# Optimization experiments

Measured on AMD Instinct MI355X. Metric: run time of the kernel, lower is better.

## Reference

```python
import jax, jax.numpy as jnp
import numpy as np

N, E = 50000, 800000
D_IN, D_HID, D_OUT = 128, 128, 64


def sage_conv(x, src, dst, w_l, w_r, b, n_nodes):
    # PyG SAGEConv (aggr='mean', root_weight=True):
    #   out = lin_l(mean_{j in N(i)} x_j) + lin_r(x_i)
    msg_sum = jax.ops.segment_sum(x[src], dst, num_segments=n_nodes)  # [N, d]
    cnt = jax.ops.segment_sum(jnp.ones((src.shape[0],), x.dtype), dst,
                              num_segments=n_nodes)                   # [N]
    mean = msg_sum / jnp.maximum(cnt, 1.0)[:, None]
    return mean @ w_l.T + x @ w_r.T + b


def prelu(x, a):
    return jnp.maximum(x, 0) + a * jnp.minimum(x, 0)


def setup_inputs() -> dict:
    key = jax.random.key(0)
    ks = jax.random.split(key, 12)
    def lin(k, o, i):
        s = 1.0 / np.sqrt(i)
        return jax.random.uniform(k, (o, i), jnp.float32, -s, s)
    x = jax.random.normal(ks[0], (N, D_IN), jnp.float32)
    edge_index = jax.random.randint(ks[1], (2, E), 0, N, jnp.int64)
    return {
        "x": x,
        "edge_index": edge_index,
        "w1l": lin(ks[2], D_HID, D_IN),  "w1r": lin(ks[3], D_HID, D_IN),
        "b1": jnp.zeros((D_HID,), jnp.float32),
        "w2l": lin(ks[4], D_HID, D_HID), "w2r": lin(ks[5], D_HID, D_HID),
        "b2": jnp.zeros((D_HID,), jnp.float32),
        "w3l": lin(ks[6], D_OUT, D_HID), "w3r": lin(ks[7], D_OUT, D_HID),
        "b3": jnp.zeros((D_OUT,), jnp.float32),
        "a": jnp.array(0.25, jnp.float32),  # shared PReLU slope
        "wp": lin(ks[8], 1, D_OUT),
        "bp": jnp.zeros((1,), jnp.float32),
    }


def reference(x, edge_index, w1l, w1r, b1, w2l, w2r, b2, w3l, w3r, b3, a, wp, bp):
    src, dst = edge_index[0], edge_index[1]
    n = x.shape[0]
    h = prelu(sage_conv(x, src, dst, w1l, w1r, b1, n), a)
    h = prelu(sage_conv(h, src, dst, w2l, w2r, b2, n), a)
    h = sage_conv(h, src, dst, w3l, w3r, b3, n)          # [N, D_OUT]
    level = (h @ wp.T + bp).squeeze(-1)                  # [N]
    return level
```

## Files before the change

### kernel.cpp

```cpp
#include <hip/hip_runtime.h>
#include <cstdint>
#include <cstddef>

typedef float f32x4 __attribute__((ext_vector_type(4)));
typedef short short8 __attribute__((ext_vector_type(8)));
typedef __bf16 bf16x8 __attribute__((ext_vector_type(8)));

__device__ __forceinline__ void mfma_bf16(f32x4& d, short8 a, short8 b){
  d = __builtin_amdgcn_mfma_f32_16x16x32_bf16(
        __builtin_bit_cast(bf16x8, a), __builtin_bit_cast(bf16x8, b), d, 0, 0, 0);
}

__device__ __forceinline__ unsigned short bf16_rn(float f){
  unsigned u = __float_as_uint(f);
  unsigned r = (u + 0x7FFF + ((u >> 16) & 1)) >> 16;
  return (unsigned short)r;
}

__device__ __forceinline__ int blockScan256Excl(int v, int* wsum){
  const int lane = threadIdx.x & 63, wv = threadIdx.x >> 6;
  int x = v;
  #pragma unroll
  for (int off = 1; off < 64; off <<= 1){
    int y = __shfl_up(x, off);
    if (lane >= off) x += y;
  }
  if (lane == 63) wsum[wv] = x;
  __syncthreads();
  int woff = 0;
  #pragma unroll
  for (int w = 0; w < 4; ++w) woff += (w < wv) ? wsum[w] : 0;
  return woff + x - v;
}

__global__ __launch_bounds__(256) void k_bcount(const int* __restrict__ dst, int E, int nb, int ntiles,
                                                int* __restrict__ blk_hist){
  __shared__ int h[256];
  const int tile = blockIdx.x;
  h[threadIdx.x] = 0;
  __syncthreads();
  const int base = tile * 2048;
  const int end = min(base + 2048, E);
  for (int i = base + threadIdx.x; i < end; i += 256)
    atomicAdd(&h[dst[i] >> 8], 1);
  __syncthreads();
  const int b = threadIdx.x;
  if (b < nb) blk_hist[(size_t)b * ntiles + tile] = h[b];
}

__global__ __launch_bounds__(256) void k_bscan(int* __restrict__ blk_hist, int nb, int ntiles,
                                               int* __restrict__ tot){
  __shared__ int wsum[4];
  __shared__ int carry;
  const int b = blockIdx.x;
  int* row = blk_hist + (size_t)b * ntiles;
  if (threadIdx.x == 0) carry = 0;
  __syncthreads();
  const int lane = threadIdx.x & 63, wv = threadIdx.x >> 6;
  for (int base = 0; base < ntiles; base += 256){
    const int i = base + threadIdx.x;
    const int v = (i < ntiles) ? row[i] : 0;
    int x = v;
    #pragma unroll
    for (int off = 1; off < 64; off <<= 1){
      int y = __shfl_up(x, off);
      if (lane >= off) x += y;
    }
    if (lane == 63) wsum[wv] = x;
    __syncthreads();
    int woff = 0;
    #pragma unroll
    for (int w = 0; w < 4; ++w) woff += (w < wv) ? wsum[w] : 0;
    const int incl = carry + woff + x;
    if (i < ntiles) row[i] = incl - v;
    __syncthreads();
    if (threadIdx.x == 255) carry = incl;
    __syncthreads();
  }
  if (threadIdx.x == 0) tot[b] = carry;
}

__global__ __launch_bounds__(256) void k_btot(const int* __restrict__ tot, int nb,
                                              int* __restrict__ bucket_base){
  __shared__ int wsum[4];
  const int t = threadIdx.x;
  const int v = (t < nb) ? tot[t] : 0;
  const int e = blockScan256Excl(v, wsum);
  if (t <= nb) bucket_base[t] = e;
}

__global__ __launch_bounds__(256) void k_bscat(const int* __restrict__ src, const int* __restrict__ dst,
                                               int E, int nb, int ntiles,
                                               const int* __restrict__ blk_off,
                                               const int* __restrict__ bucket_base,
                                               unsigned* __restrict__ ebuf){
  __shared__ int cnt[256];
  __shared__ int lofs[256];
  __shared__ int gbase[256];
  __shared__ unsigned sorted[2048];
  __shared__ unsigned char sb[2048];
  __shared__ int wsum[4];
  const int tile = blockIdx.x;
  cnt[threadIdx.x] = 0;
  __syncthreads();
  const int base = tile * 2048;
  const int end = min(base + 2048, E);
  const int m = end - base;

  int rank_[8]; int b_[8]; unsigned v_[8];
  #pragma unroll
  for (int k = 0; k < 8; ++k){
    const int j = threadIdx.x + k * 256;
    if (base + j < end){
      const int d = dst[base + j];
      const int s = src[base + j];
      const int b = d >> 8;
      b_[k] = b;
      v_[k] = ((unsigned)(d & 255) << 16) | (unsigned)s;
      rank_[k] = atomicAdd(&cnt[b], 1);
    } else b_[k] = -1;
  }
  __syncthreads();
  const int ex = blockScan256Excl(cnt[threadIdx.x], wsum);
  lofs[threadIdx.x] = ex;
  if (threadIdx.x < nb)
    gbase[threadIdx.x] = bucket_base[threadIdx.x] + blk_off[(size_t)threadIdx.x * ntiles + tile];
  __syncthreads();
  #pragma unroll
  for (int k = 0; k < 8; ++k){
    if (b_[k] >= 0){
      const int p = lofs[b_[k]] + rank_[k];
      sorted[p] = v_[k];
      sb[p] = (unsigned char)b_[k];
    }
  }
  __syncthreads();
  for (int j = threadIdx.x; j < m; j += 256){
    const int b = sb[j];
    ebuf[gbase[b] + (j - lofs[b])] = sorted[j];
  }
}

__global__ __launch_bounds__(256) void k_csrfin(const unsigned* __restrict__ ebuf,
                                                const int* __restrict__ bucket_base,
                                                int n, int E, int nb,
                                                int* __restrict__ row_ptr,
                                                float* __restrict__ inv,
                                                unsigned short* __restrict__ csr){
  __shared__ int hist[256], excl[256], cursor[256];
  __shared__ int wsum[4];
  __shared__ unsigned vals[8192];
  __shared__ unsigned short sorted[8192];
  const int b = blockIdx.x;
  const int ebase = bucket_base[b];
  const int ecnt = bucket_base[b + 1] - ebase;
  const int t = threadIdx.x;
  hist[t] = 0;
  __syncthreads();
  for (int j = t; j < ecnt; j += 256){
    const unsigned v = ebuf[ebase + j];
    vals[j] = v;
    atomicAdd(&hist[v >> 16], 1);
  }
  __syncthreads();
  const int ex = blockScan256Excl(hist[t], wsum);
  excl[t] = ex;
  cursor[t] = ex;
  const int node = b * 256 + t;
  if (node < n){
    row_ptr[node] = ebase + ex;
    const int c = hist[t];
    inv[node] = 1.0f / (float)(c > 0 ? c : 1);
  }
  if (b == nb - 1 && t == 0) row_ptr[n] = E;
  __syncthreads();
  for (int j = t; j < ecnt; j += 256){
    const unsigned v = vals[j];
    const int pos = atomicAdd(&cursor[v >> 16], 1);
    sorted[pos] = (unsigned short)(v & 0xFFFFu);
  }
  __syncthreads();
  for (int j = t; j < ecnt; j += 256)
    csr[ebase + j] = sorted[j];
}

__device__ __forceinline__ void wcs_body(const float* __restrict__ wl, const float* __restrict__ wr,
                                         short* __restrict__ bfr, int id){
  if (id >= 128 * 256) return;
  int c = id >> 8, k = id & 255;
  float w = (k < 128) ? wl[c * 128 + k] : wr[c * 128 + (k - 128)];
  unsigned short h = bf16_rn(w);
  float hf = __uint_as_float((unsigned)h << 16);
  unsigned short l = bf16_rn(w - hf);
  const int nt = c >> 4, mrow = c & 15;
  const int ks = k >> 5, kgrp = (k >> 3) & 3, j = k & 7;
  const int lane = kgrp * 16 + mrow;
  const size_t fbase = (size_t)((ks * 8 + nt) * 2) * 512 + lane * 8 + j;
  bfr[fbase] = (short)h;
  bfr[fbase + 512] = (short)l;
}

__global__ __launch_bounds__(256) void k_prep(const float* __restrict__ x,
                                              unsigned short* __restrict__ xb, int n,
                                              const float* __restrict__ w1l, const float* __restrict__ w1r,
                                              short* __restrict__ bfr1,
                                              const float* __restrict__ w2l, const float* __restrict__ w2r,
                                              short* __restrict__ bfr2,
                                              const float* __restrict__ w3l, const float* __restrict__ w3r,
                                              const float* __restrict__ b3,
                                              const float* __restrict__ wp, const float* __restrict__ bp,
                                              float* __restrict__ u){
  const int nbcvt = (n * 128 / 4 + 255) / 256;
  const int b = blockIdx.x;
  if (b < nbcvt){
    const int i = (b * 256 + threadIdx.x) * 4;
    if (i < n * 128){
      const float4 v = *(const float4*)&x[i];
      ushort2 a, c;
      a.x = bf16_rn(v.x); a.y = bf16_rn(v.y);
      c.x = bf16_rn(v.z); c.y = bf16_rn(v.w);
      *(ushort2*)&xb[i] = a;
      *(ushort2*)&xb[i + 2] = c;
    }
  } else if (b < nbcvt + 128){
    wcs_body(w1l, w1r, bfr1, (b - nbcvt) * 256 + threadIdx.x);
  } else if (b < nbcvt + 256){
    wcs_body(w2l, w2r, bfr2, (b - nbcvt - 128) * 256 + threadIdx.x);
  } else {
    const int k = threadIdx.x;
    if (k < 128){
      float sl = 0.f, sr = 0.f;
      for (int o = 0; o < 64; ++o){
        float w = wp[o];
        sl = fmaf(w, w3l[o * 128 + k], sl);
        sr = fmaf(w, w3r[o * 128 + k], sr);
      }
      u[k] = sl; u[128 + k] = sr;
      if (k == 0){
        float c = bp[0];
        for (int o = 0; o < 64; ++o) c = fmaf(wp[o], b3[o], c);
        u[256] = c;
      }
    }
  }
}

__global__ __launch_bounds__(256) void k_aggb(const unsigned short* __restrict__ featb,
                                              const unsigned short* __restrict__ csr,
                                              const int* __restrict__ row_ptr,
                                              const float* __restrict__ inv_cnt,
                                              unsigned short* __restrict__ outb, int n){
  const int lane = threadIdx.x & 63;
  const int node = (blockIdx.x * blockDim.x + threadIdx.x) >> 6;
  if (node >= n) return;
  const int beg = __builtin_amdgcn_readfirstlane(row_ptr[node]);
  const int end = __builtin_amdgcn_readfirstlane(row_ptr[node + 1]);
  const unsigned* __restrict__ fb = (const unsigned*)featb;

  float axs[8] = {0,0,0,0,0,0,0,0};
  float ays[8] = {0,0,0,0,0,0,0,0};

  int j = beg;
  for (; j + 16 <= end; j += 16){
    unsigned uu[16];
    #pragma unroll
    for (int q = 0; q < 16; ++q) uu[q] = fb[(size_t)csr[j + q] * 64 + lane];
    #pragma unroll
    for (int q = 0; q < 16; ++q){
      axs[q & 7] += __uint_as_float(uu[q] << 16);
      ays[q & 7] += __uint_as_float(uu[q] & 0xFFFF0000u);
    }
  }
  if (j + 8 <= end){
    unsigned uu[8];
    #pragma unroll
    for (int q = 0; q < 8; ++q) uu[q] = fb[(size_t)csr[j + q] * 64 + lane];
    #pragma unroll
    for (int q = 0; q < 8; ++q){
      axs[q] += __uint_as_float(uu[q] << 16);
      ays[q] += __uint_as_float(uu[q] & 0xFFFF0000u);
    }
    j += 8;
  }
  if (j + 4 <= end){
    unsigned uu[4];
    #pragma unroll
    for (int q = 0; q < 4; ++q) uu[q] = fb[(size_t)csr[j + q] * 64 + lane];
    #pragma unroll
    for (int q = 0; q < 4; ++q){
      axs[q] += __uint_as_float(uu[q] << 16);
      ays[q] += __uint_as_float(uu[q] & 0xFFFF0000u);
    }
    j += 4;
  }
  for (; j < end; ++j){
    const unsigned u = fb[(size_t)csr[j] * 64 + lane];
    axs[4] += __uint_as_float(u << 16);
    ays[4] += __uint_as_float(u & 0xFFFF0000u);
  }

  const float ic = inv_cnt[node];
  const float ox = (((axs[0] + axs[1]) + (axs[2] + axs[3])) + ((axs[4] + axs[5]) + (axs[6] + axs[7]))) * ic;
  const float oy = (((ays[0] + ays[1]) + (ays[2] + ays[3])) + ((ays[4] + ays[5]) + (ays[6] + ays[7]))) * ic;
  const unsigned packed = (unsigned)bf16_rn(ox) | ((unsigned)bf16_rn(oy) << 16);
  ((unsigned*)outb)[(size_t)node * 64 + lane] = packed;
}

__global__ __launch_bounds__(256) void k_gemm_mfma(const unsigned short* __restrict__ A0b,
                                                   const unsigned short* __restrict__ A1b,
                                                   const short* __restrict__ bfr,
                                                   const float* __restrict__ bias,
                                                   const float* __restrict__ alpha_p,
                                                   unsigned short* __restrict__ out16,
                                                   const float* __restrict__ uvec,
                                                   float* __restrict__ sbuf,
                                                   float* __restrict__ pbuf,
                                                   int n){
  __shared__ short aT[2][64 * 128];
  const int t = threadIdx.x;
  const int lane = t & 63;
  const int wv = t >> 6;
  const int nodeBase = blockIdx.x * 64;

  #pragma unroll
  for (int tab = 0; tab < 2; ++tab){
    const unsigned short* __restrict__ src = tab ? A1b : A0b;
    #pragma unroll
    for (int it = 0; it < 4; ++it){
      const int chunk = it * 256 + t;
      const int row = chunk >> 4;
      const int slot = chunk & 15;
      int gr = nodeBase + row; if (gr > n - 1) gr = n - 1;
      const uint4 v = *(const uint4*)&src[(size_t)gr * 128 + slot * 8];
      const int sslot = slot ^ (row & 7);
      *(uint4*)((char*)&aT[tab][0] + row * 256 + sslot * 16) = v;
    }
  }
  __syncthreads();

  const short8* __restrict__ Bf = (const short8*)bfr;
  const int mrow = lane & 15;
  const int kgrp = lane >> 4;
  const int arow = wv * 16 + mrow;

  f32x4 acc[8];
  #pragma unroll
  for (int i = 0; i < 8; ++i) acc[i] = (f32x4){0.f, 0.f, 0.f, 0.f};

  #pragma unroll
  for (int ks = 0; ks < 8; ++ks){
    const int tab = ks >> 2;
    const int slot_r = (ks & 3) * 4 + kgrp;
    const short8 aF = *(const short8*)((const char*)&aT[tab][0] + arow * 256 + (slot_r ^ (arow & 7)) * 16);

    short8 bh[8], bl[8];
    const int fb = ks * 16;
    #pragma unroll
    for (int nt = 0; nt < 8; ++nt){
      bh[nt] = Bf[(size_t)(fb + nt * 2 + 0) * 64 + lane];
      bl[nt] = Bf[(size_t)(fb + nt * 2 + 1) * 64 + lane];
    }
    #pragma unroll
    for (int nt = 0; nt < 8; ++nt){
      mfma_bf16(acc[nt], aF, bh[nt]);
      mfma_bf16(acc[nt], aF, bl[nt]);
    }
  }

  const float alpha = *alpha_p;
  const int nodeQ = nodeBase + wv * 16 + kgrp * 4;

  if (out16){
    #pragma unroll
    for (int nt = 0; nt < 8; ++nt){
      const int col = nt * 16 + mrow;
      const float bv = bias[col];
      #pragma unroll
      for (int j = 0; j < 4; ++j){
        const int onode = nodeQ + j;
        if (onode < n){
          float v = acc[nt][j] + bv;
          v = fmaxf(v, 0.f) + alpha * fminf(v, 0.f);
          out16[(size_t)onode * 128 + col] = bf16_rn(v);
        }
      }
    }
  } else {
    float sdot[4] = {0,0,0,0}, tdot[4] = {0,0,0,0};
    #pragma unroll
    for (int nt = 0; nt < 8; ++nt){
      const int col = nt * 16 + mrow;
      const float bv = bias[col];
      const float ul = uvec[col];
      const float ur = uvec[128 + col];
      #pragma unroll
      for (int j = 0; j < 4; ++j){
        float v = acc[nt][j] + bv;
        v = fmaxf(v, 0.f) + alpha * fminf(v, 0.f);
        sdot[j] = fmaf(v, ul, sdot[j]);
        tdot[j] = fmaf(v, ur, tdot[j]);
      }
    }
    #pragma unroll
    for (int j = 0; j < 4; ++j){
      #pragma unroll
      for (int off = 1; off < 16; off <<= 1){
        sdot[j] += __shfl_xor(sdot[j], off);
        tdot[j] += __shfl_xor(tdot[j], off);
      }
    }
    if (mrow == 0){
      const float c = uvec[256];
      #pragma unroll
      for (int j = 0; j < 4; ++j){
        const int onode = nodeQ + j;
        if (onode < n){
          sbuf[onode] = sdot[j];
          pbuf[onode] = tdot[j] + c;
        }
      }
    }
  }
}

__global__ __launch_bounds__(256) void k_final(const float* __restrict__ s, const float* __restrict__ partial,
                        const unsigned short* __restrict__ csr, const int* __restrict__ row_ptr,
                        const float* __restrict__ inv_cnt, float* __restrict__ out, int n){
  const int t = blockIdx.x * blockDim.x + threadIdx.x;
  const int node = t >> 2;
  const int sub = t & 3;
  if (node >= n) return;
  const int b = row_ptr[node], e = row_ptr[node + 1];
  float a0 = 0.f, a1 = 0.f;
  int j = b + sub;
  for (; j + 4 < e; j += 8){
    a0 += s[csr[j]];
    a1 += s[csr[j + 4]];
  }
  if (j < e) a0 += s[csr[j]];
  float acc = a0 + a1;
  acc += __shfl_down(acc, 1);
  acc += __shfl_down(acc, 2);
  if (sub == 0) out[node] = acc * inv_cnt[node] + partial[node];
}

extern "C" void kernel_launch(void* const* d_in, const int* in_sizes, int n_in,
                              void* d_out, int out_size, void* d_ws, size_t ws_size,
                              hipStream_t stream){
  const float* x   = (const float*)d_in[0];
  const int*   ei  = (const int*)d_in[1];
  const float* w1l = (const float*)d_in[2];
  const float* w1r = (const float*)d_in[3];
  const float* b1  = (const float*)d_in[4];
  const float* w2l = (const float*)d_in[5];
  const float* w2r = (const float*)d_in[6];
  const float* b2  = (const float*)d_in[7];
  const float* w3l = (const float*)d_in[8];
  const float* w3r = (const float*)d_in[9];
  const float* b3  = (const float*)d_in[10];
  const float* ap  = (const float*)d_in[11];
  const float* wp  = (const float*)d_in[12];
  const float* bp  = (const float*)d_in[13];

  const int n = out_size;
  const int E = in_sizes[1] / 2;
  const int* srcI = ei;
  const int* dstI = ei + E;

  const int ntiles = (E + 2047) / 2048;
  const int nb = (n + 255) >> 8;

  char* base = (char*)d_ws;
  size_t off = 0;
  auto take = [&](size_t bytes) -> char* {
    off = (off + 255) & ~(size_t)255;
    char* p = base + off;
    off += bytes;
    return p;
  };
  int*      blk_hist = (int*)   take((size_t)nb * ntiles * 4);
  int*      tot      = (int*)   take((size_t)nb * 4);
  int*      bbase    = (int*)   take(((size_t)nb + 1) * 4);
  unsigned* ebuf     = (unsigned*)take((size_t)E * 4);
  int*      rowp     = (int*)   take(((size_t)n + 1) * 4);
  float*    inv      = (float*) take((size_t)n * 4);
  unsigned short* csr = (unsigned short*)take((size_t)E * 2);
  unsigned short* B1b = (unsigned short*)take((size_t)n * 128 * 2);
  unsigned short* xb  = (unsigned short*)take((size_t)n * 128 * 2);
  unsigned short* h1b = (unsigned short*)take((size_t)n * 128 * 2);
  float*    sbuf = (float*)take((size_t)n * 4);
  float*    pbuf = (float*)take((size_t)n * 4);
  float*    u    = (float*)take(257 * 4);
  short*    bfr1 = (short*)take((size_t)128 * 512 * 2);
  short*    bfr2 = (short*)take((size_t)128 * 512 * 2);
  (void)ws_size; (void)n_in;

  k_bcount<<<ntiles, 256, 0, stream>>>(dstI, E, nb, ntiles, blk_hist);
  k_bscan <<<nb,     256, 0, stream>>>(blk_hist, nb, ntiles, tot);
  k_btot  <<<1,      256, 0, stream>>>(tot, nb, bbase);
  k_bscat <<<ntiles, 256, 0, stream>>>(srcI, dstI, E, nb, ntiles, blk_hist, bbase, ebuf);
  k_csrfin<<<nb,     256, 0, stream>>>(ebuf, bbase, n, E, nb, rowp, inv, csr);

  const int nbcvt = (n * 128 / 4 + 255) / 256;
  k_prep<<<nbcvt + 257, 256, 0, stream>>>(x, xb, n, w1l, w1r, bfr1, w2l, w2r, bfr2,
                                          w3l, w3r, b3, wp, bp, u);

  const int aggGrid  = (n * 64 + 255) / 256;
  const int gemmGrid = (n + 63) / 64;

  k_aggb     <<<aggGrid, 256, 0, stream>>>(xb, csr, rowp, inv, B1b, n);
  k_gemm_mfma<<<gemmGrid, 256, 0, stream>>>(B1b, xb, bfr1, b1, ap, h1b,
                                            (const float*)nullptr, (float*)nullptr, (float*)nullptr, n);

  k_aggb     <<<aggGrid, 256, 0, stream>>>(h1b, csr, rowp, inv, B1b, n);
  k_gemm_mfma<<<gemmGrid, 256, 0, stream>>>(B1b, h1b, bfr2, b2, ap, (unsigned short*)nullptr,
                                            u, sbuf, pbuf, n);

  k_final<<<(n * 4 + 255) / 256, 256, 0, stream>>>(sbuf, pbuf, csr, rowp, inv, (float*)d_out, n);
}
```

Before: 156.0 us.

## Fold bucket-total scan into scatter/finalize kernels and double GEMM rows per block

Removes the single-block k_btot launch by having k_bscat and k_csrfin each recompute the exclusive scan of bucket totals locally, which saves one kernel launch and a serial dependency. Separately, the MFMA GEMM now handles 128 nodes per block instead of 64, with each wave computing two 16-row tiles so every loaded B fragment is reused twice. This halves the grid and the B-fragment global traffic per node. The cost is double the LDS (64KB) and accumulator registers, which may reduce occupancy.

```diff
diff --git a/kernel.cpp b/kernel.cpp
--- a/kernel.cpp
+++ b/kernel.cpp
@@ -80,19 +80,11 @@
   if (threadIdx.x == 0) tot[b] = carry;
 }
 
-__global__ __launch_bounds__(256) void k_btot(const int* __restrict__ tot, int nb,
-                                              int* __restrict__ bucket_base){
-  __shared__ int wsum[4];
-  const int t = threadIdx.x;
-  const int v = (t < nb) ? tot[t] : 0;
-  const int e = blockScan256Excl(v, wsum);
-  if (t <= nb) bucket_base[t] = e;
-}
 
 __global__ __launch_bounds__(256) void k_bscat(const int* __restrict__ src, const int* __restrict__ dst,
                                                int E, int nb, int ntiles,
                                                const int* __restrict__ blk_off,
-                                               const int* __restrict__ bucket_base,
+                                               const int* __restrict__ tot,
                                                unsigned* __restrict__ ebuf){
   __shared__ int cnt[256];
   __shared__ int lofs[256];
@@ -123,8 +115,11 @@
   __syncthreads();
   const int ex = blockScan256Excl(cnt[threadIdx.x], wsum);
   lofs[threadIdx.x] = ex;
+  __syncthreads();
+  const int tvv = (threadIdx.x < nb) ? tot[threadIdx.x] : 0;
+  const int bb0 = blockScan256Excl(tvv, wsum);
   if (threadIdx.x < nb)
-    gbase[threadIdx.x] = bucket_base[threadIdx.x] + blk_off[(size_t)threadIdx.x * ntiles + tile];
+    gbase[threadIdx.x] = bb0 + blk_off[(size_t)threadIdx.x * ntiles + tile];
   __syncthreads();
   #pragma unroll
   for (int k = 0; k < 8; ++k){
@@ -142,21 +137,25 @@
 }
 
 __global__ __launch_bounds__(256) void k_csrfin(const unsigned* __restrict__ ebuf,
-                                                const int* __restrict__ bucket_base,
+                                                const int* __restrict__ tot,
                                                 int n, int E, int nb,
                                                 int* __restrict__ row_ptr,
                                                 float* __restrict__ inv,
                                                 unsigned short* __restrict__ csr){
-  __shared__ int hist[256], excl[256], cursor[256];
+  __shared__ int hist[256], cursor[256], bbs[257];
   __shared__ int wsum[4];
   __shared__ unsigned vals[8192];
   __shared__ unsigned short sorted[8192];
   const int b = blockIdx.x;
-  const int ebase = bucket_base[b];
-  const int ecnt = bucket_base[b + 1] - ebase;
   const int t = threadIdx.x;
+  const int tvv = (t < nb) ? tot[t] : 0;
+  const int bb0 = blockScan256Excl(tvv, wsum);
+  bbs[t] = bb0;
+  if (t == 255) bbs[256] = bb0 + tvv;
   hist[t] = 0;
   __syncthreads();
+  const int ebase = bbs[b];
+  const int ecnt = bbs[b + 1] - ebase;
   for (int j = t; j < ecnt; j += 256){
     const unsigned v = ebuf[ebase + j];
     vals[j] = v;
@@ -164,7 +163,6 @@
   }
   __syncthreads();
   const int ex = blockScan256Excl(hist[t], wsum);
-  excl[t] = ex;
   cursor[t] = ex;
   const int node = b * 256 + t;
   if (node < n){
@@ -316,17 +314,17 @@
                                                    float* __restrict__ sbuf,
                                                    float* __restrict__ pbuf,
                                                    int n){
-  __shared__ short aT[2][64 * 128];
+  __shared__ short aT[2][128 * 128];
   const int t = threadIdx.x;
   const int lane = t & 63;
   const int wv = t >> 6;
-  const int nodeBase = blockIdx.x * 64;
+  const int nodeBase = blockIdx.x * 128;
 
   #pragma unroll
   for (int tab = 0; tab < 2; ++tab){
     const unsigned short* __restrict__ src = tab ? A1b : A0b;
     #pragma unroll
-    for (int it = 0; it < 4; ++it){
+    for (int it = 0; it < 8; ++it){
       const int chunk = it * 256 + t;
       const int row = chunk >> 4;
       const int slot = chunk & 15;
@@ -341,17 +339,21 @@
   const short8* __restrict__ Bf = (const short8*)bfr;
   const int mrow = lane & 15;
   const int kgrp = lane >> 4;
-  const int arow = wv * 16 + mrow;
-
-  f32x4 acc[8];
-  #pragma unroll
-  for (int i = 0; i < 8; ++i) acc[i] = (f32x4){0.f, 0.f, 0.f, 0.f};
+  const int arow0 = wv * 32 + mrow;
+  const int arow1 = arow0 + 16;
+
+  f32x4 acc[2][8];
+  #pragma unroll
+  for (int s = 0; s < 2; ++s)
+    #pragma unroll
+    for (int i = 0; i < 8; ++i) acc[s][i] = (f32x4){0.f, 0.f, 0.f, 0.f};
 
   #pragma unroll
   for (int ks = 0; ks < 8; ++ks){
     const int tab = ks >> 2;
     const int slot_r = (ks & 3) * 4 + kgrp;
-    const short8 aF = *(const short8*)((const char*)&aT[tab][0] + arow * 256 + (slot_r ^ (arow & 7)) * 16);
+    const short8 aF0 = *(const short8*)((const char*)&aT[tab][0] + arow0 * 256 + (slot_r ^ (arow0 & 7)) * 16);
+    const short8 aF1 = *(const short8*)((const char*)&aT[tab][0] + arow1 * 256 + (slot_r ^ (arow1 & 7)) * 16);
 
     short8 bh[8], bl[8];
     const int fb = ks * 16;
@@ -362,61 +364,70 @@
     }
     #pragma unroll
     for (int nt = 0; nt < 8; ++nt){
-      mfma_bf16(acc[nt], aF, bh[nt]);
-      mfma_bf16(acc[nt], aF, bl[nt]);
+      mfma_bf16(acc[0][nt], aF0, bh[nt]);
+      mfma_bf16(acc[0][nt], aF0, bl[nt]);
+      mfma_bf16(acc[1][nt], aF1, bh[nt]);
+      mfma_bf16(acc[1][nt], aF1, bl[nt]);
     }
   }
 
   const float alpha = *alpha_p;
-  const int nodeQ = nodeBase + wv * 16 + kgrp * 4;
 
   if (out16){
     #pragma unroll
-    for (int nt = 0; nt < 8; ++nt){
-      const int col = nt * 16 + mrow;
-      const float bv = bias[col];
+    for (int s = 0; s < 2; ++s){
+      const int nodeQ = nodeBase + wv * 32 + s * 16 + kgrp * 4;
+      #pragma unroll
+      for (int nt = 0; nt < 8; ++nt){
+        const int col = nt * 16 + mrow;
+        const float bv = bias[col];
+        #pragma unroll
+        for (int j = 0; j < 4; ++j){
+          const int onode = nodeQ + j;
+          if (onode < n){
+            float v = acc[s][nt][j] + bv;
+            v = fmaxf(v, 0.f) + alpha * fminf(v, 0.f);
+            out16[(size_t)onode * 128 + col] = bf16_rn(v);
+          }
+        }
+      }
+    }
+  } else {
+    #pragma unroll
+    for (int s = 0; s < 2; ++s){
+      float sdot[4] = {0,0,0,0}, tdot[4] = {0,0,0,0};
+      #pragma unroll
+      for (int nt = 0; nt < 8; ++nt){
+        const int col = nt * 16 + mrow;
+        const float bv = bias[col];
+        const float ul = uvec[col];
+        const float ur = uvec[128 + col];
+        #pragma unroll
+        for (int j = 0; j < 4; ++j){
+          float v = acc[s][nt][j] + bv;
+          v = fmaxf(v, 0.f) + alpha * fminf(v, 0.f);
+          sdot[j] = fmaf(v, ul, sdot[j]);
+          tdot[j] = fmaf(v, ur, tdot[j]);
+        }
+      }
       #pragma unroll
       for (int j = 0; j < 4; ++j){
-        const int onode = nodeQ + j;
-        if (onode < n){
-          float v = acc[nt][j] + bv;
-          v = fmaxf(v, 0.f) + alpha * fminf(v, 0.f);
-          out16[(size_t)onode * 128 + col] = bf16_rn(v);
+        #pragma unroll
+        for (int off = 1; off < 16; off <<= 1){
+          sdot[j] += __shfl_xor(sdot[j], off);
+          tdot[j] += __shfl_xor(tdot[j], off);
         }
       }
-    }
-  } else {
-    float sdot[4] = {0,0,0,0}, tdot[4] = {0,0,0,0};
-    #pragma unroll
-    for (int nt = 0; nt < 8; ++nt){
-      const int col = nt * 16 + mrow;
-      const float bv = bias[col];
-      const float ul = uvec[col];
-      const float ur = uvec[128 + col];
-      #pragma unroll
-      for (int j = 0; j < 4; ++j){
-        float v = acc[nt][j] + bv;
-        v = fmaxf(v, 0.f) + alpha * fminf(v, 0.f);
-        sdot[j] = fmaf(v, ul, sdot[j]);
-        tdot[j] = fmaf(v, ur, tdot[j]);
-      }
-    }
-    #pragma unroll
-    for (int j = 0; j < 4; ++j){
-      #pragma unroll
-      for (int off = 1; off < 16; off <<= 1){
-        sdot[j] += __shfl_xor(sdot[j], off);
-        tdot[j] += __shfl_xor(tdot[j], off);
-      }
-    }
-    if (mrow == 0){
-      const float c = uvec[256];
-      #pragma unroll
-      for (int j = 0; j < 4; ++j){
-        const int onode = nodeQ + j;
-        if (onode < n){
-          sbuf[onode] = sdot[j];
-          pbuf[onode] = tdot[j] + c;
+      if (mrow == 0){
+        const float c = uvec[256];
+        const int nodeQ = nodeBase + wv * 32 + s * 16 + kgrp * 4;
+        #pragma unroll
+        for (int j = 0; j < 4; ++j){
+          const int onode = nodeQ + j;
+          if (onode < n){
+            sbuf[onode] = sdot[j];
+            pbuf[onode] = tdot[j] + c;
+          }
         }
       }
     }
@@ -480,7 +491,6 @@
   };
   int*      blk_hist = (int*)   take((size_t)nb * ntiles * 4);
   int*      tot      = (int*)   take((size_t)nb * 4);
-  int*      bbase    = (int*)   take(((size_t)nb + 1) * 4);
   unsigned* ebuf     = (unsigned*)take((size_t)E * 4);
   int*      rowp     = (int*)   take(((size_t)n + 1) * 4);
   float*    inv      = (float*) take((size_t)n * 4);
@@ -497,16 +507,15 @@
 
   k_bcount<<<ntiles, 256, 0, stream>>>(dstI, E, nb, ntiles, blk_hist);
   k_bscan <<<nb,     256, 0, stream>>>(blk_hist, nb, ntiles, tot);
-  k_btot  <<<1,      256, 0, stream>>>(tot, nb, bbase);
-  k_bscat <<<ntiles, 256, 0, stream>>>(srcI, dstI, E, nb, ntiles, blk_hist, bbase, ebuf);
-  k_csrfin<<<nb,     256, 0, stream>>>(ebuf, bbase, n, E, nb, rowp, inv, csr);
+  k_bscat <<<ntiles, 256, 0, stream>>>(srcI, dstI, E, nb, ntiles, blk_hist, tot, ebuf);
+  k_csrfin<<<nb,     256, 0, stream>>>(ebuf, tot, n, E, nb, rowp, inv, csr);
 
   const int nbcvt = (n * 128 / 4 + 255) / 256;
   k_prep<<<nbcvt + 257, 256, 0, stream>>>(x, xb, n, w1l, w1r, bfr1, w2l, w2r, bfr2,
                                           w3l, w3r, b3, wp, bp, u);
 
   const int aggGrid  = (n * 64 + 255) / 256;
-  const int gemmGrid = (n + 63) / 64;
+  const int gemmGrid = (n + 127) / 128;
 
   k_aggb     <<<aggGrid, 256, 0, stream>>>(xb, csr, rowp, inv, B1b, n);
   k_gemm_mfma<<<gemmGrid, 256, 0, stream>>>(B1b, xb, bfr1, b1, ap, h1b,
```

New measurement: 157.1 us. About the same (+0.7%).
